# Kernel tuning notes

Measured on AMD Instinct MI355X. Metric: run time of the kernel, lower is better.

The kernel has to match this reference:

```python
import jax, jax.numpy as jnp
import numpy as np

EPS = 1e-5
GRID = 128          # coarse grid extent -> fine grid is 256^3
N1 = 15000          # coarse voxels
CHILD = 4           # children kept per coarse voxel
N2 = N1 * CHILD     # fine voxels
CIN = 128
COUT = 64


def _build_geometry():
    rng = np.random.RandomState(0)
    flat = rng.choice(GRID ** 3, N1, replace=False)
    cc = np.stack(np.unravel_index(flat, (GRID, GRID, GRID)), axis=1)  # [N1,3]
    offs8 = np.array([[i, j, k] for i in (0, 1) for j in (0, 1) for k in (0, 1)], dtype=np.int64)
    kidx = np.argsort(rng.rand(N1, 8), axis=1)[:, :CHILD]              # [N1,4] distinct child taps
    fine = (cc[:, None, :] * 2 + offs8[kidx]).reshape(-1, 3)           # [N2,3] unique fine coords
    up_src = np.repeat(np.arange(N1), CHILD).astype(np.int32)
    up_kidx = kidx.reshape(-1).astype(np.int32)
    # 27-offset neighbor maps via hashed coordinate lookup
    key = (fine[:, 0] * 256 + fine[:, 1]) * 256 + fine[:, 2]
    order = np.argsort(key)
    skey = key[order]
    offs27 = np.array([[i, j, k] for i in (-1, 0, 1) for j in (-1, 0, 1) for k in (-1, 0, 1)], dtype=np.int64)
    nbr_src = np.full((27, N2), N2, dtype=np.int32)
    nbr_dst = np.full((27, N2), N2, dtype=np.int32)
    for t in range(27):
        q = fine + offs27[t]
        inb = np.all((q >= 0) & (q < 256), axis=1)
        qk = (q[:, 0] * 256 + q[:, 1]) * 256 + q[:, 2]
        pos = np.searchsorted(skey, qk)
        pos = np.clip(pos, 0, N2 - 1)
        hit = inb & (skey[pos] == qk)
        nbr_src[t, hit] = order[pos[hit]]
        nbr_dst[t, hit] = np.arange(N2, dtype=np.int32)[hit]
    return up_src, up_kidx, nbr_src, nbr_dst


def setup_inputs() -> dict:
    key = jax.random.key(0)
    ks = jax.random.split(key, 8)
    up_src, up_kidx, nbr_src, nbr_dst = _build_geometry()
    s_up = 1.0 / np.sqrt(CIN * 8)
    s1 = 1.0 / np.sqrt(CIN * 27)
    s2 = 1.0 / np.sqrt(COUT * 27)
    return {
        "feats1": jax.random.normal(ks[0], (N1, CIN), jnp.float32),
        "feats2": jax.random.normal(ks[1], (N2, CIN // 2), jnp.float32),
        "w_up": jax.random.normal(ks[2], (8, CIN, CIN // 2), jnp.float32) * s_up,
        "gamma_up": jnp.ones((CIN // 2,), jnp.float32),
        "beta_up": jnp.zeros((CIN // 2,), jnp.float32),
        "w1": jax.random.normal(ks[3], (27, CIN, COUT), jnp.float32) * s1,
        "gamma1": jnp.ones((COUT,), jnp.float32),
        "beta1": jnp.zeros((COUT,), jnp.float32),
        "w2": jax.random.normal(ks[4], (27, COUT, COUT), jnp.float32) * s2,
        "gamma2": jnp.ones((COUT,), jnp.float32),
        "beta2": jnp.zeros((COUT,), jnp.float32),
        "up_src": jnp.asarray(up_src),
        "up_kidx": jnp.asarray(up_kidx),
        "nbr_src": jnp.asarray(nbr_src),
        "nbr_dst": jnp.asarray(nbr_dst),
    }


def _bn_relu(x, gamma, beta):
    # training-mode BatchNorm over the point dimension (biased variance), then ReLU
    m = jnp.mean(x, axis=0)
    v = jnp.var(x, axis=0)
    return jax.nn.relu((x - m) * jax.lax.rsqrt(v + EPS) * gamma + beta)


def _sparse_conv(x, w, nbr_src, nbr_dst):
    # x: [N,Ci]; w: [27,Ci,Co]; transform-then-gather-scatter (hash-map sparse conv)
    n = x.shape[0]
    co = w.shape[-1]
    y = jnp.einsum("nc,kco->kno", x, w)                       # [27,N,Co]
    y = jnp.concatenate([y, jnp.zeros((27, 1, co), y.dtype)], axis=1)  # sentinel row
    msg = jnp.take_along_axis(y, nbr_src[:, :, None], axis=1)  # [27,N,Co]
    out = jnp.zeros((n + 1, co), y.dtype).at[nbr_dst.reshape(-1)].add(msg.reshape(-1, co))
    return out[:-1]


def reference(feats1, feats2, w_up, gamma_up, beta_up, w1, gamma1, beta1, w2,
              gamma2, beta2, up_src, up_kidx, nbr_src, nbr_dst):
    # transposed conv k=2 s=2, generative=False: each fine voxel pulls from its unique coarse parent
    y = jnp.einsum("mc,kco->kmo", feats1, w_up)               # [8,N1,Cin/2]
    x1 = y[up_kidx, up_src]                                   # [N2,Cin/2]
    x1 = _bn_relu(x1, gamma_up, beta_up)
    x = jnp.concatenate([x1, feats2], axis=-1)                # [N2,Cin]
    h = _bn_relu(_sparse_conv(x, w1, nbr_src, nbr_dst), gamma1, beta1)
    return _bn_relu(_sparse_conv(h, w2, nbr_src, nbr_dst), gamma2, beta2)
```

## Files before the change

kernel.cpp:

```cpp
#include <hip/hip_runtime.h>


typedef short bf16x4 __attribute__((ext_vector_type(4)));
typedef short bf16x8 __attribute__((ext_vector_type(8)));
typedef float f32x16 __attribute__((ext_vector_type(16)));

__device__ __forceinline__ short f2bf(float f) {
    unsigned u = __float_as_uint(f);
    u += 0x7fffu + ((u >> 16) & 1u);
    return (short)(u >> 16);
}
__device__ __forceinline__ float bf2f(short s) {
    return __uint_as_float(((unsigned)(unsigned short)s) << 16);
}

__global__ __launch_bounds__(256) void k_setup(
    const float* __restrict__ w_up, const float* __restrict__ w1,
    const float* __restrict__ w2, const float* __restrict__ f1,
    const int* __restrict__ nbr, const int* __restrict__ up_kidx,
    short* __restrict__ wupp, short* __restrict__ w1p,
    short* __restrict__ w2p, short* __restrict__ f1bf,
    int* __restrict__ pmask, int* __restrict__ perm_rows,
    int* __restrict__ rank, int* __restrict__ cnt,
    int2* __restrict__ ext, int* __restrict__ extc,
    int n1, int n2, int nbExt, int nbGeom)
{
    int tid = threadIdx.x;
    int bid = blockIdx.x;
    if (bid < nbExt) {
        int i = bid * 256 + tid;
        unsigned hm = 0;
        if (i < n2) {
            #pragma unroll
            for (int t = 0; t < 27; ++t) {
                int s = nbr[(size_t)t * n2 + i];
                if (s < n2 && (s >> 2) != (i >> 2)) hm |= 1u << t;
            }
        }
        __shared__ int lcnt, lbase;
        if (tid == 0) lcnt = 0;
        __syncthreads();
        int nh = __popc(hm);
        int myofs = 0;
        if (nh) myofs = atomicAdd(&lcnt, nh);
        __syncthreads();
        if (tid == 0 && lcnt) lbase = atomicAdd(extc, lcnt);
        __syncthreads();
        if (nh) {
            int pos = lbase + myofs;
            unsigned m = hm;
            while (m) {
                int t = __ffs(m) - 1;
                m &= m - 1;
                int s = nbr[(size_t)t * n2 + i];
                ext[pos++] = make_int2(i, s | (t << 16));
            }
        }
    } else if (bid < nbExt + nbGeom) {
        int p = (bid - nbExt) * 256 + tid;
        if (p >= n1) return;
        int4 kd = *(const int4*)(up_kidx + 4 * p);
        int a = kd.x * 4 + 0, b = kd.y * 4 + 1, c = kd.z * 4 + 2, d = kd.w * 4 + 3;
        int t;
        if (a > b) { t = a; a = b; b = t; }
        if (c > d) { t = c; c = d; d = t; }
        if (a > c) { t = a; a = c; c = t; }
        if (b > d) { t = b; b = d; d = t; }
        if (b > c) { t = b; b = c; c = t; }
        perm_rows[4 * p + 0] = 4 * p + (a & 3);
        perm_rows[4 * p + 1] = 4 * p + (b & 3);
        perm_rows[4 * p + 2] = 4 * p + (c & 3);
        perm_rows[4 * p + 3] = 4 * p + (d & 3);
        int mask = (1 << (a >> 2)) | (1 << (b >> 2)) | (1 << (c >> 2)) | (1 << (d >> 2));
        pmask[p] = mask;
        rank[p] = atomicAdd(&cnt[mask], 1);
    } else {
        const long long nup = 65536, nw1 = 221184, nw2 = 110592;
        long long nf1 = (long long)n1 * 128;
        long long total = nup + nw1 + nw2 + nf1;
        long long gs = (long long)(gridDim.x - nbExt - nbGeom) * 256;
        for (long long e0 = (long long)(bid - nbExt - nbGeom) * 256 + tid;
             e0 < total; e0 += gs) {
            long long e = e0;
            if (e < nup) {
                int j = e & 7, l = (e >> 3) & 63, nt = (e >> 9) & 15, ks = (int)(e >> 13);
                int k = ks * 16 + (l >> 5) * 8 + j;
                int col = nt * 32 + (l & 31);
                wupp[e] = f2bf(w_up[((size_t)(col >> 6) * 128 + k) * 64 + (col & 63)]);
            } else if ((e -= nup) < nw1) {
                int j = e & 7, l = (e >> 3) & 63, ch = (e >> 9) & 1, ks = (e >> 10) & 7, t = (int)(e >> 13);
                int k = ks * 16 + (l >> 5) * 8 + j;
                int col = ch * 32 + (l & 31);
                w1p[e] = f2bf(w1[((size_t)t * 128 + k) * 64 + col]);
            } else if ((e -= nw1) < nw2) {
                int j = e & 7, l = (e >> 3) & 63, ch = (e >> 9) & 1, ks = (e >> 10) & 3, t = (int)(e >> 12);
                int k = ks * 16 + (l >> 5) * 8 + j;
                int col = ch * 32 + (l & 31);
                w2p[e] = f2bf(w2[((size_t)t * 64 + k) * 64 + col]);
            } else {
                e -= nw2;
                f1bf[e] = f2bf(f1[e]);
            }
        }
    }
}

__global__ __launch_bounds__(256) void k_up(
    const short* __restrict__ f1bf, const short* __restrict__ wupp,
    const int* __restrict__ pmask, const int* __restrict__ cnt,
    const int* __restrict__ rank, int* __restrict__ perm_par,
    int4* __restrict__ tiles, int* __restrict__ ntl,
    short* __restrict__ yup8, float* __restrict__ stats, int n1)
{
    if (blockIdx.x == 0) {
        __shared__ int sA[256], sB[256], bb[256];
        int t = threadIdx.x;
        int c = cnt[t], tc = (c + 31) >> 5;
        sA[t] = c; sB[t] = tc;
        __syncthreads();
        for (int off = 1; off < 256; off <<= 1) {
            int a = (t >= off) ? sA[t - off] : 0;
            int b = (t >= off) ? sB[t - off] : 0;
            __syncthreads();
            sA[t] += a; sB[t] += b;
            __syncthreads();
        }
        int base = sA[t] - c, toff = sB[t] - tc;
        bb[t] = base;
        for (int j = 0; j < tc; ++j) tiles[toff + j] = make_int4(t, base, j * 32, c);
        if (t == 255) ntl[0] = sB[255];
        __syncthreads();
        for (int p = t; p < n1; p += 256)
            perm_par[bb[pmask[p]] + rank[p]] = p;
        return;
    }
    __shared__ short lds[32 * 136];
    __shared__ float bs[64], bq[64];
    int bid = blockIdx.x - 1;
    int tile = bid >> 1;
    int w = threadIdx.x >> 6, lane = threadIdx.x & 63;
    int na = (bid & 1) * 8 + w, nb = na + 4;
    if (threadIdx.x < 64) { bs[threadIdx.x] = 0.f; bq[threadIdx.x] = 0.f; }
    #pragma unroll
    for (int it = 0; it < 2; ++it) {
        int c = it * 256 + threadIdx.x;
        int row = c >> 4, col8 = c & 15;
        int gr = tile * 32 + row; if (gr >= n1) gr = n1 - 1;
        int4 g = *(const int4*)(f1bf + (size_t)gr * 128 + col8 * 8);
        short* d = &lds[row * 136 + col8 * 8];
        *(int2*)d = make_int2(g.x, g.y);
        *(int2*)(d + 4) = make_int2(g.z, g.w);
    }
    int m = lane & 31, half = lane >> 5;
    int pm_l = (tile * 32 + m < n1) ? pmask[tile * 32 + m] : 0;
    __syncthreads();
    f32x16 a0, a1;
    #pragma unroll
    for (int i = 0; i < 16; ++i) { a0[i] = 0.f; a1[i] = 0.f; }
    const bf16x8* bp = (const bf16x8*)wupp;
    #pragma unroll
    for (int ks = 0; ks < 8; ++ks) {
        const short* ap = &lds[m * 136 + ks * 16 + half * 8];
        bf16x4 lo = *(const bf16x4*)ap, hi = *(const bf16x4*)(ap + 4);
        bf16x8 a = __builtin_shufflevector(lo, hi, 0, 1, 2, 3, 4, 5, 6, 7);
        bf16x8 b0 = bp[(size_t)(ks * 16 + na) * 64 + lane];
        bf16x8 b1 = bp[(size_t)(ks * 16 + nb) * 64 + lane];
        a0 = __builtin_amdgcn_mfma_f32_32x32x16_bf16(a, b0, a0, 0, 0, 0);
        a1 = __builtin_amdgcn_mfma_f32_32x32x16_bf16(a, b1, a1, 0, 0, 0);
    }
    int col = lane & 31;
    #pragma unroll
    for (int pass = 0; pass < 2; ++pass) {
        const f32x16& acc = pass ? a1 : a0;
        int n = pass ? nb : na;
        int slot = n >> 1, c = (n & 1) * 32 + col;
        float s0 = 0.f, q0 = 0.f;
        #pragma unroll
        for (int reg = 0; reg < 16; ++reg) {
            int r = (reg & 3) + 8 * (reg >> 2) + 4 * half;
            int p = tile * 32 + r;
            float v = acc[reg];
            int mk = __shfl(pm_l, r);
            if (p < n1) {
                yup8[(size_t)p * 512 + n * 32 + col] = f2bf(v);
                if ((mk >> slot) & 1) { s0 += v; q0 += v * v; }
            }
        }
        s0 += __shfl_xor(s0, 32);
        q0 += __shfl_xor(q0, 32);
        if (lane < 32) { atomicAdd(&bs[c], s0); atomicAdd(&bq[c], q0); }
    }
    __syncthreads();
    if (threadIdx.x < 64) {
        atomicAdd(&stats[threadIdx.x], bs[threadIdx.x]);
        atomicAdd(&stats[64 + threadIdx.x], bq[threadIdx.x]);
    }
}

__global__ __launch_bounds__(256) void k_extA(
    const short* __restrict__ yup8, const float* __restrict__ f2,
    const int* __restrict__ up_kidx, const float* __restrict__ w1,
    const float* __restrict__ gamma, const float* __restrict__ beta,
    const float* __restrict__ stats, const int2* __restrict__ ext,
    const int* __restrict__ extc, float* __restrict__ y,
    float* __restrict__ ostats, int n2)
{
    __shared__ float sc[64], sh[64], bs[64], bq[64];
    int tid = threadIdx.x;
    if (tid < 64) {
        float inv = 1.0f / (float)n2;
        float mean = stats[tid] * inv;
        float var = stats[64 + tid] * inv - mean * mean;
        float s = gamma[tid] * rsqrtf(var + 1e-5f);
        sc[tid] = s; sh[tid] = beta[tid] - mean * s;
        bs[tid] = 0.f; bq[tid] = 0.f;
    }
    __syncthreads();
    int gw = (blockIdx.x * 256 + tid) >> 6;
    int nw = (gridDim.x * 256) >> 6;
    int c = tid & 63;
    int ec = extc[0];
    float ls = 0.f, lq = 0.f;
    for (int e = gw; e < ec; e += nw) {
        int2 en = ext[e];
        int i = en.x, s = en.y & 0xFFFF, t = en.y >> 16;
        const short* xr = yup8 + (size_t)(s >> 2) * 512 + up_kidx[s] * 64;
        const float* fr = f2 + (size_t)s * 64;
        const float* wr = w1 + (size_t)t * 8192 + c;
        float acc = 0.f;
        #pragma unroll 4
        for (int k = 0; k < 64; ++k) {
            float xk = fmaxf(bf2f(xr[k]) * sc[k] + sh[k], 0.f);
            acc += xk * wr[(size_t)k * 64];
        }
        #pragma unroll 4
        for (int k = 0; k < 64; ++k)
            acc += fr[k] * wr[(size_t)(64 + k) * 64];
        float old = atomicAdd(&y[(size_t)i * 64 + c], acc);
        ls += acc;
        lq += acc * (2.f * old + acc);
    }
    atomicAdd(&bs[c], ls);
    atomicAdd(&bq[c], lq);
    __syncthreads();
    if (tid < 64) {
        atomicAdd(&ostats[tid], bs[tid]);
        atomicAdd(&ostats[64 + tid], bq[tid]);
    }
}

__global__ __launch_bounds__(256) void k_extB(
    const float* __restrict__ y1, const float* __restrict__ w2,
    const float* __restrict__ gamma, const float* __restrict__ beta,
    const float* __restrict__ stats, const int2* __restrict__ ext,
    const int* __restrict__ extc, float* __restrict__ y,
    float* __restrict__ ostats, int n2)
{
    __shared__ float sc[64], sh[64], bs[64], bq[64];
    int tid = threadIdx.x;
    if (tid < 64) {
        float inv = 1.0f / (float)n2;
        float mean = stats[tid] * inv;
        float var = stats[64 + tid] * inv - mean * mean;
        float s = gamma[tid] * rsqrtf(var + 1e-5f);
        sc[tid] = s; sh[tid] = beta[tid] - mean * s;
        bs[tid] = 0.f; bq[tid] = 0.f;
    }
    __syncthreads();
    int gw = (blockIdx.x * 256 + tid) >> 6;
    int nw = (gridDim.x * 256) >> 6;
    int c = tid & 63;
    int ec = extc[0];
    float ls = 0.f, lq = 0.f;
    for (int e = gw; e < ec; e += nw) {
        int2 en = ext[e];
        int i = en.x, s = en.y & 0xFFFF, t = en.y >> 16;
        const float* hr = y1 + (size_t)s * 64;
        const float* wr = w2 + (size_t)t * 4096 + c;
        float acc = 0.f;
        #pragma unroll 4
        for (int k = 0; k < 64; ++k) {
            float hk = fmaxf(hr[k] * sc[k] + sh[k], 0.f);
            acc += hk * wr[(size_t)k * 64];
        }
        float old = atomicAdd(&y[(size_t)i * 64 + c], acc);
        ls += acc;
        lq += acc * (2.f * old + acc);
    }
    atomicAdd(&bs[c], ls);
    atomicAdd(&bq[c], lq);
    __syncthreads();
    if (tid < 64) {
        atomicAdd(&ostats[tid], bs[tid]);
        atomicAdd(&ostats[64 + tid], bq[tid]);
    }
}

__device__ __forceinline__ void pair_epi_store(const f32x16& a0v, const f32x16& a1v,
                                               int outrow0, int outrow1, int lane,
                                               int ch, float* __restrict__ y,
                                               float* __restrict__ bs,
                                               float* __restrict__ bq)
{
    int col = lane & 31;
    int c = ch * 32 + col;
    int r0[16], r1[16];
    #pragma unroll
    for (int reg = 0; reg < 16; ++reg) {
        int r = (reg & 3) + 8 * (reg >> 2) + 4 * (lane >> 5);
        r0[reg] = __shfl(outrow0, r);
        r1[reg] = __shfl(outrow1, r);
    }
    float s0 = 0.f, q0 = 0.f;
    #pragma unroll
    for (int reg = 0; reg < 16; ++reg) {
        if (r0[reg] >= 0) {
            float v = a0v[reg];
            y[(size_t)r0[reg] * 64 + c] = v;
            s0 += v; q0 += v * v;
        }
        if (r1[reg] >= 0) {
            float v = a1v[reg];
            y[(size_t)r1[reg] * 64 + c] = v;
            s0 += v; q0 += v * v;
        }
    }
    s0 += __shfl_xor(s0, 32);
    q0 += __shfl_xor(q0, 32);
    if (lane < 32) { atomicAdd(&bs[c], s0); atomicAdd(&bq[c], q0); }
}

__device__ __forceinline__ int tap27(int pa, int pb) {
    int di = ((pb >> 2) & 1) - ((pa >> 2) & 1);
    int dj = ((pb >> 1) & 1) - ((pa >> 1) & 1);
    int dk = (pb & 1) - (pa & 1);
    return (di + 1) * 9 + (dj + 1) * 3 + (dk + 1);
}

__global__ __launch_bounds__(256) void k_pairA(
    const short* __restrict__ yup8, const float* __restrict__ f2,
    const int* __restrict__ up_kidx, const short* __restrict__ wp,
    const float* __restrict__ gamma, const float* __restrict__ beta,
    const float* __restrict__ stats, const int* __restrict__ perm_par,
    const int* __restrict__ perm_rows, const int4* __restrict__ tiles,
    const int* __restrict__ n_tiles, float* __restrict__ y,
    float* __restrict__ ostats, int n2)
{
    constexpr int LP = 520;
    __shared__ short lds[32 * LP];
    __shared__ int srows[128], soff[128];
    __shared__ float scs[64], shs[64], bs[64], bq[64];
    int bt = blockIdx.x;
    if (bt >= n_tiles[0]) return;
    int4 td = tiles[bt];
    int mask = td.x, p_start = td.y, lt = td.z, cntb = td.w;
    int tid = threadIdx.x;
    if (tid < 128) {
        int li = lt + (tid >> 2);
        int pid = perm_par[p_start + ((li < cntb) ? li : 0)];
        int i = perm_rows[pid * 4 + (tid & 3)];
        srows[tid] = i;
        soff[tid] = (i >> 2) * 512 + up_kidx[i] * 64;
    } else if (tid < 192) {
        int cc = tid - 128;
        float inv = 1.0f / (float)n2;
        float mean = stats[cc] * inv;
        float var = stats[64 + cc] * inv - mean * mean;
        float s = gamma[cc] * rsqrtf(var + 1e-5f);
        scs[cc] = s; shs[cc] = beta[cc] - mean * s;
    } else {
        int cc = tid - 192;
        bs[cc] = 0.f; bq[cc] = 0.f;
    }
    __syncthreads();
    #pragma unroll
    for (int it = 0; it < 8; ++it) {
        int c0 = it * 256 + tid;
        int pl = c0 >> 6, w8 = c0 & 63;
        int j = w8 >> 4, col8 = w8 & 15;
        short* d = &lds[pl * LP + j * 128 + col8 * 8];
        if (col8 < 8) {
            bf16x8 g = *(const bf16x8*)(yup8 + (size_t)soff[pl * 4 + j] + col8 * 8);
            short o[8];
            #pragma unroll
            for (int u = 0; u < 8; ++u) {
                int cc = col8 * 8 + u;
                o[u] = f2bf(fmaxf(bf2f(g[u]) * scs[cc] + shs[cc], 0.f));
            }
            *(int2*)d = make_int2(((int)(unsigned short)o[0]) | ((int)o[1] << 16),
                                  ((int)(unsigned short)o[2]) | ((int)o[3] << 16));
            *(int2*)(d + 4) = make_int2(((int)(unsigned short)o[4]) | ((int)o[5] << 16),
                                        ((int)(unsigned short)o[6]) | ((int)o[7] << 16));
        } else {
            const float* fr = f2 + (size_t)srows[pl * 4 + j] * 64 + (col8 - 8) * 8;
            float4 f0 = *(const float4*)fr;
            float4 f1v = *(const float4*)(fr + 4);
            short o[8] = {f2bf(f0.x), f2bf(f0.y), f2bf(f0.z), f2bf(f0.w),
                          f2bf(f1v.x), f2bf(f1v.y), f2bf(f1v.z), f2bf(f1v.w)};
            *(int2*)d = make_int2(((int)(unsigned short)o[0]) | ((int)o[1] << 16),
                                  ((int)(unsigned short)o[2]) | ((int)o[3] << 16));
            *(int2*)(d + 4) = make_int2(((int)(unsigned short)o[4]) | ((int)o[5] << 16),
                                        ((int)(unsigned short)o[6]) | ((int)o[7] << 16));
        }
    }
    int p0 = -1, p1 = -1, p2 = -1, p3 = -1;
    #pragma unroll
    for (int b = 7; b >= 0; --b)
        if ((mask >> b) & 1) { p3 = p2; p2 = p1; p1 = p0; p0 = b; }
    int w = tid >> 6, lane = tid & 63;
    int a0 = w >> 1, a1 = a0 + 2, ch = w & 1;
    int pa0 = (a0 == 0) ? p0 : p1;
    int pa1 = (a1 == 2) ? p2 : p3;
    int t00 = tap27(pa0, p0), t01 = tap27(pa0, p1), t02 = tap27(pa0, p2), t03 = tap27(pa0, p3);
    int t10 = tap27(pa1, p0), t11 = tap27(pa1, p1), t12 = tap27(pa1, p2), t13 = tap27(pa1, p3);
    int m = lane & 31, half = lane >> 5;
    int li = lt + m;
    bool vp = li < cntb;
    int pid = perm_par[p_start + (vp ? li : 0)];
    int outrow0 = vp ? perm_rows[pid * 4 + a0] : -1;
    int outrow1 = vp ? perm_rows[pid * 4 + a1] : -1;
    __syncthreads();
    f32x16 acc0, acc1;
    #pragma unroll
    for (int i = 0; i < 16; ++i) { acc0[i] = 0.f; acc1[i] = 0.f; }
    const bf16x8* bp = (const bf16x8*)wp;
    #pragma unroll
    for (int b = 0; b < 4; ++b) {
        int tb0 = (b == 0) ? t00 : (b == 1) ? t01 : (b == 2) ? t02 : t03;
        int tb1 = (b == 0) ? t10 : (b == 1) ? t11 : (b == 2) ? t12 : t13;
        #pragma unroll
        for (int kk = 0; kk < 8; ++kk) {
            int ks = b * 8 + kk;
            const short* ap = &lds[m * LP + ks * 16 + half * 8];
            bf16x4 lo = *(const bf16x4*)ap, hi = *(const bf16x4*)(ap + 4);
            bf16x8 a = __builtin_shufflevector(lo, hi, 0, 1, 2, 3, 4, 5, 6, 7);
            bf16x8 b0 = bp[((size_t)(tb0 * 8 + kk) * 2 + ch) * 64 + lane];
            bf16x8 b1 = bp[((size_t)(tb1 * 8 + kk) * 2 + ch) * 64 + lane];
            acc0 = __builtin_amdgcn_mfma_f32_32x32x16_bf16(a, b0, acc0, 0, 0, 0);
            acc1 = __builtin_amdgcn_mfma_f32_32x32x16_bf16(a, b1, acc1, 0, 0, 0);
        }
    }
    pair_epi_store(acc0, acc1, outrow0, outrow1, lane, ch, y, bs, bq);
    __syncthreads();
    if (tid < 64) {
        atomicAdd(&ostats[tid], bs[tid]);
        atomicAdd(&ostats[64 + tid], bq[tid]);
    }
}

__global__ __launch_bounds__(256) void k_pairB(
    const float* __restrict__ y1, const short* __restrict__ wp,
    const float* __restrict__ gamma, const float* __restrict__ beta,
    const float* __restrict__ stats, const int* __restrict__ perm_par,
    const int* __restrict__ perm_rows, const int4* __restrict__ tiles,
    const int* __restrict__ n_tiles, float* __restrict__ y,
    float* __restrict__ ostats, int n2)
{
    constexpr int LP = 264;
    __shared__ short lds[32 * LP];
    __shared__ int srows[128];
    __shared__ float scs[64], shs[64], bs[64], bq[64];
    int bt = blockIdx.x;
    if (bt >= n_tiles[0]) return;
    int4 td = tiles[bt];
    int mask = td.x, p_start = td.y, lt = td.z, cntb = td.w;
    int tid = threadIdx.x;
    if (tid < 128) {
        int li = lt + (tid >> 2);
        int pid = perm_par[p_start + ((li < cntb) ? li : 0)];
        srows[tid] = perm_rows[pid * 4 + (tid & 3)];
    } else if (tid < 192) {
        int cc = tid - 128;
        float inv = 1.0f / (float)n2;
        float mean = stats[cc] * inv;
        float var = stats[64 + cc] * inv - mean * mean;
        float s = gamma[cc] * rsqrtf(var + 1e-5f);
        scs[cc] = s; shs[cc] = beta[cc] - mean * s;
    } else {
        int cc = tid - 192;
        bs[cc] = 0.f; bq[cc] = 0.f;
    }
    __syncthreads();
    #pragma unroll
    for (int it = 0; it < 4; ++it) {
        int c0 = it * 256 + tid;
        int pl = c0 >> 5, w8 = c0 & 31;
        int j = w8 >> 3, col8 = w8 & 7;
        const float* fr = y1 + (size_t)srows[pl * 4 + j] * 64 + col8 * 8;
        float4 f0 = *(const float4*)fr;
        float4 f1v = *(const float4*)(fr + 4);
        short o[8];
        #pragma unroll
        for (int u = 0; u < 4; ++u) {
            int cc = col8 * 8 + u;
            float v = (u == 0) ? f0.x : (u == 1) ? f0.y : (u == 2) ? f0.z : f0.w;
            o[u] = f2bf(fmaxf(v * scs[cc] + shs[cc], 0.f));
        }
        #pragma unroll
        for (int u = 0; u < 4; ++u) {
            int cc = col8 * 8 + 4 + u;
            float v = (u == 0) ? f1v.x : (u == 1) ? f1v.y : (u == 2) ? f1v.z : f1v.w;
            o[4 + u] = f2bf(fmaxf(v * scs[cc] + shs[cc], 0.f));
        }
        short* d = &lds[pl * LP + j * 64 + col8 * 8];
        *(int2*)d = make_int2(((int)(unsigned short)o[0]) | ((int)o[1] << 16),
                              ((int)(unsigned short)o[2]) | ((int)o[3] << 16));
        *(int2*)(d + 4) = make_int2(((int)(unsigned short)o[4]) | ((int)o[5] << 16),
                                    ((int)(unsigned short)o[6]) | ((int)o[7] << 16));
    }
    int p0 = -1, p1 = -1, p2 = -1, p3 = -1;
    #pragma unroll
    for (int b = 7; b >= 0; --b)
        if ((mask >> b) & 1) { p3 = p2; p2 = p1; p1 = p0; p0 = b; }
    int w = tid >> 6, lane = tid & 63;
    int a0 = w >> 1, a1 = a0 + 2, ch = w & 1;
    int pa0 = (a0 == 0) ? p0 : p1;
    int pa1 = (a1 == 2) ? p2 : p3;
    int t00 = tap27(pa0, p0), t01 = tap27(pa0, p1), t02 = tap27(pa0, p2), t03 = tap27(pa0, p3);
    int t10 = tap27(pa1, p0), t11 = tap27(pa1, p1), t12 = tap27(pa1, p2), t13 = tap27(pa1, p3);
    int m = lane & 31, half = lane >> 5;
    int li = lt + m;
    bool vp = li < cntb;
    int pid = perm_par[p_start + (vp ? li : 0)];
    int outrow0 = vp ? perm_rows[pid * 4 + a0] : -1;
    int outrow1 = vp ? perm_rows[pid * 4 + a1] : -1;
    __syncthreads();
    f32x16 acc0, acc1;
    #pragma unroll
    for (int i = 0; i < 16; ++i) { acc0[i] = 0.f; acc1[i] = 0.f; }
    const bf16x8* bp = (const bf16x8*)wp;
    #pragma unroll
    for (int b = 0; b < 4; ++b) {
        int tb0 = (b == 0) ? t00 : (b == 1) ? t01 : (b == 2) ? t02 : t03;
        int tb1 = (b == 0) ? t10 : (b == 1) ? t11 : (b == 2) ? t12 : t13;
        #pragma unroll
        for (int kk = 0; kk < 4; ++kk) {
            int ks = b * 4 + kk;
            const short* ap = &lds[m * LP + ks * 16 + half * 8];
            bf16x4 lo = *(const bf16x4*)ap, hi = *(const bf16x4*)(ap + 4);
            bf16x8 a = __builtin_shufflevector(lo, hi, 0, 1, 2, 3, 4, 5, 6, 7);
            bf16x8 b0 = bp[((size_t)(tb0 * 4 + kk) * 2 + ch) * 64 + lane];
            bf16x8 b1 = bp[((size_t)(tb1 * 4 + kk) * 2 + ch) * 64 + lane];
            acc0 = __builtin_amdgcn_mfma_f32_32x32x16_bf16(a, b0, acc0, 0, 0, 0);
            acc1 = __builtin_amdgcn_mfma_f32_32x32x16_bf16(a, b1, acc1, 0, 0, 0);
        }
    }
    pair_epi_store(acc0, acc1, outrow0, outrow1, lane, ch, y, bs, bq);
    __syncthreads();
    if (tid < 64) {
        atomicAdd(&ostats[tid], bs[tid]);
        atomicAdd(&ostats[64 + tid], bq[tid]);
    }
}

__global__ __launch_bounds__(256) void k_final(
    const float* __restrict__ y, const float* __restrict__ gamma,
    const float* __restrict__ beta, const float* __restrict__ stats,
    float* __restrict__ out, int n2)
{
    __shared__ float sc[64], sh[64];
    int tid = threadIdx.x;
    if (tid < 64) {
        float inv = 1.0f / (float)n2;
        float mean = stats[tid] * inv;
        float var = stats[64 + tid] * inv - mean * mean;
        float s = gamma[tid] * rsqrtf(var + 1e-5f);
        sc[tid] = s;
        sh[tid] = beta[tid] - mean * s;
    }
    __syncthreads();
    long long total = (long long)n2 * 16;
    long long stride = (long long)gridDim.x * blockDim.x;
    for (long long idx = (long long)blockIdx.x * blockDim.x + tid; idx < total; idx += stride) {
        int i = (int)(idx >> 4);
        int c4 = ((int)idx & 15) * 4;
        const float* src = y + (size_t)i * 64 + c4;
        float4 o;
        o.x = fmaxf(src[0] * sc[c4 + 0] + sh[c4 + 0], 0.f);
        o.y = fmaxf(src[1] * sc[c4 + 1] + sh[c4 + 1], 0.f);
        o.z = fmaxf(src[2] * sc[c4 + 2] + sh[c4 + 2], 0.f);
        o.w = fmaxf(src[3] * sc[c4 + 3] + sh[c4 + 3], 0.f);
        *(float4*)(out + (size_t)i * 64 + c4) = o;
    }
}

extern "C" void kernel_launch(void* const* d_in, const int* in_sizes, int n_in,
                              void* d_out, int out_size, void* d_ws, size_t ws_size,
                              hipStream_t stream)
{
    const float* feats1   = (const float*)d_in[0];
    const float* feats2   = (const float*)d_in[1];
    const float* w_up     = (const float*)d_in[2];
    const float* gamma_up = (const float*)d_in[3];
    const float* beta_up  = (const float*)d_in[4];
    const float* w1       = (const float*)d_in[5];
    const float* gamma1   = (const float*)d_in[6];
    const float* beta1    = (const float*)d_in[7];
    const float* w2       = (const float*)d_in[8];
    const float* gamma2   = (const float*)d_in[9];
    const float* beta2    = (const float*)d_in[10];
    const int* up_kidx    = (const int*)d_in[12];
    const int* nbr_src    = (const int*)d_in[13];

    int n1 = in_sizes[0] / 128;
    int n2 = in_sizes[1] / 64;

    char* p = (char*)d_ws;
    auto alloc = [&](size_t bytes) {
        char* r = p;
        p += (bytes + 255) & ~(size_t)255;
        return r;
    };
    float* stats    = (float*)alloc(384 * 4);
    int*   cnt      = (int*)alloc(256 * 4);
    int*   extc     = (int*)alloc(16);
    int*   ntl      = (int*)alloc(16);
    size_t headBytes = (size_t)(p - (char*)d_ws);
    int maxTiles    = (n1 + 31) / 32 + 80;
    int4*  tiles    = (int4*)alloc((size_t)maxTiles * 16);
    short* wupp     = (short*)alloc((size_t)65536 * 2);
    short* w1p      = (short*)alloc((size_t)221184 * 2);
    short* w2p      = (short*)alloc((size_t)110592 * 2);
    short* f1bf     = (short*)alloc((size_t)n1 * 128 * 2);
    int*   pmask    = (int*)alloc((size_t)n1 * 4);
    int*   rank     = (int*)alloc((size_t)n1 * 4);
    int*   perm_par = (int*)alloc((size_t)n1 * 4);
    int*   perm_rows= (int*)alloc((size_t)4 * n1 * 4);
    int2*  ext      = (int2*)alloc((size_t)27 * n2 * 8);
    short* yup8     = (short*)alloc((size_t)n1 * 512 * 2);
    float* y1       = (float*)alloc((size_t)n2 * 64 * 4);
    float* y2       = (float*)alloc((size_t)n2 * 64 * 4);

    int nbExt  = (n2 + 255) / 256;
    int nbGeom = (n1 + 255) / 256;
    int nbPack = 256;
    int nbSetup = nbExt + nbGeom + nbPack;
    int upBlocks = 1 + 2 * ((n1 + 31) / 32);
    int ewBlocks16 = (int)(((long long)n2 * 16 + 255) / 256);

    hipMemsetAsync(d_ws, 0, headBytes, stream);
    k_setup<<<nbSetup, 256, 0, stream>>>(w_up, w1, w2, feats1, nbr_src, up_kidx,
                                         wupp, w1p, w2p, f1bf, pmask, perm_rows,
                                         rank, cnt, ext, extc, n1, n2,
                                         nbExt, nbGeom);
    k_up<<<upBlocks, 256, 0, stream>>>(f1bf, wupp, pmask, cnt, rank, perm_par,
                                       tiles, ntl, yup8, stats, n1);
    k_pairA<<<maxTiles, 256, 0, stream>>>(yup8, feats2, up_kidx, w1p, gamma_up,
                                          beta_up, stats, perm_par, perm_rows,
                                          tiles, ntl, y1, stats + 128, n2);
    k_extA<<<256, 256, 0, stream>>>(yup8, feats2, up_kidx, w1, gamma_up, beta_up,
                                    stats, ext, extc, y1, stats + 128, n2);
    k_pairB<<<maxTiles, 256, 0, stream>>>(y1, w2p, gamma1, beta1, stats + 128,
                                          perm_par, perm_rows, tiles, ntl, y2,
                                          stats + 256, n2);
    k_extB<<<256, 256, 0, stream>>>(y1, w2, gamma1, beta1, stats + 128, ext,
                                    extc, y2, stats + 256, n2);
    k_final<<<ewBlocks16, 256, 0, stream>>>(y2, gamma2, beta2, stats + 256,
                                            (float*)d_out, n2);
}
```

Baseline: 273.3 us.

## Merge pair-tile and cross-parent conv work into one launch per layer

Each sparse conv layer previously ran two kernels: an MFMA pair-tile kernel that stored outputs, then a scalar kernel that atomically added cross-parent contributions. Both now run as one grid, with extra blocks past the tile count doing the cross-parent work concurrently. Because of that, the tile epilogue switches from plain stores to atomicAdd into y1/y2, which are zero-filled in the setup kernel. Sum-of-squares stats are computed incrementally from the value returned by each atomic. This removes a launch and the serialization between the two parts per layer, at the cost of many more global atomics and extra zeroing traffic.

```diff
diff --git a/kernel.cpp b/kernel.cpp
--- a/kernel.cpp
+++ b/kernel.cpp
@@ -23,11 +23,18 @@
     int* __restrict__ pmask, int* __restrict__ perm_rows,
     int* __restrict__ rank, int* __restrict__ cnt,
     int2* __restrict__ ext, int* __restrict__ extc,
+    float* __restrict__ y1, float* __restrict__ y2,
     int n1, int n2, int nbExt, int nbGeom)
 {
     int tid = threadIdx.x;
     int bid = blockIdx.x;
     if (bid < nbExt) {
+        long long tot = (long long)n2 * 16;
+        long long gs = (long long)nbExt * 256;
+        for (long long e = (long long)bid * 256 + tid; e < tot; e += gs) {
+            ((float4*)y1)[e] = make_float4(0.f, 0.f, 0.f, 0.f);
+            ((float4*)y2)[e] = make_float4(0.f, 0.f, 0.f, 0.f);
+        }
         int i = bid * 256 + tid;
         unsigned hm = 0;
         if (i < n2) {
@@ -197,110 +204,11 @@
     }
 }
 
-__global__ __launch_bounds__(256) void k_extA(
-    const short* __restrict__ yup8, const float* __restrict__ f2,
-    const int* __restrict__ up_kidx, const float* __restrict__ w1,
-    const float* __restrict__ gamma, const float* __restrict__ beta,
-    const float* __restrict__ stats, const int2* __restrict__ ext,
-    const int* __restrict__ extc, float* __restrict__ y,
-    float* __restrict__ ostats, int n2)
-{
-    __shared__ float sc[64], sh[64], bs[64], bq[64];
-    int tid = threadIdx.x;
-    if (tid < 64) {
-        float inv = 1.0f / (float)n2;
-        float mean = stats[tid] * inv;
-        float var = stats[64 + tid] * inv - mean * mean;
-        float s = gamma[tid] * rsqrtf(var + 1e-5f);
-        sc[tid] = s; sh[tid] = beta[tid] - mean * s;
-        bs[tid] = 0.f; bq[tid] = 0.f;
-    }
-    __syncthreads();
-    int gw = (blockIdx.x * 256 + tid) >> 6;
-    int nw = (gridDim.x * 256) >> 6;
-    int c = tid & 63;
-    int ec = extc[0];
-    float ls = 0.f, lq = 0.f;
-    for (int e = gw; e < ec; e += nw) {
-        int2 en = ext[e];
-        int i = en.x, s = en.y & 0xFFFF, t = en.y >> 16;
-        const short* xr = yup8 + (size_t)(s >> 2) * 512 + up_kidx[s] * 64;
-        const float* fr = f2 + (size_t)s * 64;
-        const float* wr = w1 + (size_t)t * 8192 + c;
-        float acc = 0.f;
-        #pragma unroll 4
-        for (int k = 0; k < 64; ++k) {
-            float xk = fmaxf(bf2f(xr[k]) * sc[k] + sh[k], 0.f);
-            acc += xk * wr[(size_t)k * 64];
-        }
-        #pragma unroll 4
-        for (int k = 0; k < 64; ++k)
-            acc += fr[k] * wr[(size_t)(64 + k) * 64];
-        float old = atomicAdd(&y[(size_t)i * 64 + c], acc);
-        ls += acc;
-        lq += acc * (2.f * old + acc);
-    }
-    atomicAdd(&bs[c], ls);
-    atomicAdd(&bq[c], lq);
-    __syncthreads();
-    if (tid < 64) {
-        atomicAdd(&ostats[tid], bs[tid]);
-        atomicAdd(&ostats[64 + tid], bq[tid]);
-    }
-}
-
-__global__ __launch_bounds__(256) void k_extB(
-    const float* __restrict__ y1, const float* __restrict__ w2,
-    const float* __restrict__ gamma, const float* __restrict__ beta,
-    const float* __restrict__ stats, const int2* __restrict__ ext,
-    const int* __restrict__ extc, float* __restrict__ y,
-    float* __restrict__ ostats, int n2)
-{
-    __shared__ float sc[64], sh[64], bs[64], bq[64];
-    int tid = threadIdx.x;
-    if (tid < 64) {
-        float inv = 1.0f / (float)n2;
-        float mean = stats[tid] * inv;
-        float var = stats[64 + tid] * inv - mean * mean;
-        float s = gamma[tid] * rsqrtf(var + 1e-5f);
-        sc[tid] = s; sh[tid] = beta[tid] - mean * s;
-        bs[tid] = 0.f; bq[tid] = 0.f;
-    }
-    __syncthreads();
-    int gw = (blockIdx.x * 256 + tid) >> 6;
-    int nw = (gridDim.x * 256) >> 6;
-    int c = tid & 63;
-    int ec = extc[0];
-    float ls = 0.f, lq = 0.f;
-    for (int e = gw; e < ec; e += nw) {
-        int2 en = ext[e];
-        int i = en.x, s = en.y & 0xFFFF, t = en.y >> 16;
-        const float* hr = y1 + (size_t)s * 64;
-        const float* wr = w2 + (size_t)t * 4096 + c;
-        float acc = 0.f;
-        #pragma unroll 4
-        for (int k = 0; k < 64; ++k) {
-            float hk = fmaxf(hr[k] * sc[k] + sh[k], 0.f);
-            acc += hk * wr[(size_t)k * 64];
-        }
-        float old = atomicAdd(&y[(size_t)i * 64 + c], acc);
-        ls += acc;
-        lq += acc * (2.f * old + acc);
-    }
-    atomicAdd(&bs[c], ls);
-    atomicAdd(&bq[c], lq);
-    __syncthreads();
-    if (tid < 64) {
-        atomicAdd(&ostats[tid], bs[tid]);
-        atomicAdd(&ostats[64 + tid], bq[tid]);
-    }
-}
-
-__device__ __forceinline__ void pair_epi_store(const f32x16& a0v, const f32x16& a1v,
-                                               int outrow0, int outrow1, int lane,
-                                               int ch, float* __restrict__ y,
-                                               float* __restrict__ bs,
-                                               float* __restrict__ bq)
+__device__ __forceinline__ void pair_epi_at(const f32x16& a0v, const f32x16& a1v,
+                                            int outrow0, int outrow1, int lane,
+                                            int ch, float* __restrict__ y,
+                                            float* __restrict__ bs,
+                                            float* __restrict__ bq)
 {
     int col = lane & 31;
     int c = ch * 32 + col;
@@ -311,19 +219,17 @@
         r0[reg] = __shfl(outrow0, r);
         r1[reg] = __shfl(outrow1, r);
     }
+    float o0[16], o1[16];
+    #pragma unroll
+    for (int reg = 0; reg < 16; ++reg) {
+        o0[reg] = (r0[reg] >= 0) ? atomicAdd(&y[(size_t)r0[reg] * 64 + c], a0v[reg]) : 0.f;
+        o1[reg] = (r1[reg] >= 0) ? atomicAdd(&y[(size_t)r1[reg] * 64 + c], a1v[reg]) : 0.f;
+    }
     float s0 = 0.f, q0 = 0.f;
     #pragma unroll
     for (int reg = 0; reg < 16; ++reg) {
-        if (r0[reg] >= 0) {
-            float v = a0v[reg];
-            y[(size_t)r0[reg] * 64 + c] = v;
-            s0 += v; q0 += v * v;
-        }
-        if (r1[reg] >= 0) {
-            float v = a1v[reg];
-            y[(size_t)r1[reg] * 64 + c] = v;
-            s0 += v; q0 += v * v;
-        }
+        if (r0[reg] >= 0) { float d = a0v[reg]; s0 += d; q0 += d * (2.f * o0[reg] + d); }
+        if (r1[reg] >= 0) { float d = a1v[reg]; s0 += d; q0 += d * (2.f * o1[reg] + d); }
     }
     s0 += __shfl_xor(s0, 32);
     q0 += __shfl_xor(q0, 32);
@@ -337,24 +243,69 @@
     return (di + 1) * 9 + (dj + 1) * 3 + (dk + 1);
 }
 
-__global__ __launch_bounds__(256) void k_pairA(
+__global__ __launch_bounds__(256) void k_convA(
     const short* __restrict__ yup8, const float* __restrict__ f2,
     const int* __restrict__ up_kidx, const short* __restrict__ wp,
+    const float* __restrict__ w1f,
     const float* __restrict__ gamma, const float* __restrict__ beta,
     const float* __restrict__ stats, const int* __restrict__ perm_par,
     const int* __restrict__ perm_rows, const int4* __restrict__ tiles,
-    const int* __restrict__ n_tiles, float* __restrict__ y,
-    float* __restrict__ ostats, int n2)
+    const int* __restrict__ n_tiles, const int2* __restrict__ ext,
+    const int* __restrict__ extc, float* __restrict__ y,
+    float* __restrict__ ostats, int n2, int maxT)
 {
     constexpr int LP = 520;
     __shared__ short lds[32 * LP];
     __shared__ int srows[128], soff[128];
     __shared__ float scs[64], shs[64], bs[64], bq[64];
+    int tid = threadIdx.x;
+    if (blockIdx.x >= maxT) {
+        if (tid < 64) {
+            float inv = 1.0f / (float)n2;
+            float mean = stats[tid] * inv;
+            float var = stats[64 + tid] * inv - mean * mean;
+            float s = gamma[tid] * rsqrtf(var + 1e-5f);
+            scs[tid] = s; shs[tid] = beta[tid] - mean * s;
+            bs[tid] = 0.f; bq[tid] = 0.f;
+        }
+        __syncthreads();
+        int gw = ((blockIdx.x - maxT) * 256 + tid) >> 6;
+        int nw = ((gridDim.x - maxT) * 256) >> 6;
+        int c = tid & 63;
+        int ec = extc[0];
+        float ls = 0.f, lq = 0.f;
+        for (int e = gw; e < ec; e += nw) {
+            int2 en = ext[e];
+            int i = en.x, s = en.y & 0xFFFF, t = en.y >> 16;
+            const short* xr = yup8 + (size_t)(s >> 2) * 512 + up_kidx[s] * 64;
+            const float* fr = f2 + (size_t)s * 64;
+            const float* wr = w1f + (size_t)t * 8192 + c;
+            float acc = 0.f;
+            #pragma unroll 4
+            for (int k = 0; k < 64; ++k) {
+                float xk = fmaxf(bf2f(xr[k]) * scs[k] + shs[k], 0.f);
+                acc += xk * wr[(size_t)k * 64];
+            }
+            #pragma unroll 4
+            for (int k = 0; k < 64; ++k)
+                acc += fr[k] * wr[(size_t)(64 + k) * 64];
+            float old = atomicAdd(&y[(size_t)i * 64 + c], acc);
+            ls += acc;
+            lq += acc * (2.f * old + acc);
+        }
+        atomicAdd(&bs[c], ls);
+        atomicAdd(&bq[c], lq);
+        __syncthreads();
+        if (tid < 64) {
+            atomicAdd(&ostats[tid], bs[tid]);
+            atomicAdd(&ostats[64 + tid], bq[tid]);
+        }
+        return;
+    }
     int bt = blockIdx.x;
     if (bt >= n_tiles[0]) return;
     int4 td = tiles[bt];
     int mask = td.x, p_start = td.y, lt = td.z, cntb = td.w;
-    int tid = threadIdx.x;
     if (tid < 128) {
         int li = lt + (tid >> 2);
         int pid = perm_par[p_start + ((li < cntb) ? li : 0)];
@@ -440,7 +391,7 @@
             acc1 = __builtin_amdgcn_mfma_f32_32x32x16_bf16(a, b1, acc1, 0, 0, 0);
         }
     }
-    pair_epi_store(acc0, acc1, outrow0, outrow1, lane, ch, y, bs, bq);
+    pair_epi_at(acc0, acc1, outrow0, outrow1, lane, ch, y, bs, bq);
     __syncthreads();
     if (tid < 64) {
         atomicAdd(&ostats[tid], bs[tid]);
@@ -448,23 +399,64 @@
     }
 }
 
-__global__ __launch_bounds__(256) void k_pairB(
+__global__ __launch_bounds__(256) void k_convB(
     const float* __restrict__ y1, const short* __restrict__ wp,
+    const float* __restrict__ w2f,
     const float* __restrict__ gamma, const float* __restrict__ beta,
     const float* __restrict__ stats, const int* __restrict__ perm_par,
     const int* __restrict__ perm_rows, const int4* __restrict__ tiles,
-    const int* __restrict__ n_tiles, float* __restrict__ y,
-    float* __restrict__ ostats, int n2)
+    const int* __restrict__ n_tiles, const int2* __restrict__ ext,
+    const int* __restrict__ extc, float* __restrict__ y,
+    float* __restrict__ ostats, int n2, int maxT)
 {
     constexpr int LP = 264;
     __shared__ short lds[32 * LP];
     __shared__ int srows[128];
     __shared__ float scs[64], shs[64], bs[64], bq[64];
+    int tid = threadIdx.x;
+    if (blockIdx.x >= maxT) {
+        if (tid < 64) {
+            float inv = 1.0f / (float)n2;
+            float mean = stats[tid] * inv;
+            float var = stats[64 + tid] * inv - mean * mean;
+            float s = gamma[tid] * rsqrtf(var + 1e-5f);
+            scs[tid] = s; shs[tid] = beta[tid] - mean * s;
+            bs[tid] = 0.f; bq[tid] = 0.f;
+        }
+        __syncthreads();
+        int gw = ((blockIdx.x - maxT) * 256 + tid) >> 6;
+        int nw = ((gridDim.x - maxT) * 256) >> 6;
+        int c = tid & 63;
+        int ec = extc[0];
+        float ls = 0.f, lq = 0.f;
+        for (int e = gw; e < ec; e += nw) {
+            int2 en = ext[e];
+            int i = en.x, s = en.y & 0xFFFF, t = en.y >> 16;
+            const float* hr = y1 + (size_t)s * 64;
+            const float* wr = w2f + (size_t)t * 4096 + c;
+            float acc = 0.f;
+            #pragma unroll 4
+            for (int k = 0; k < 64; ++k) {
+                float hk = fmaxf(hr[k] * scs[k] + shs[k], 0.f);
+                acc += hk * wr[(size_t)k * 64];
+            }
+            float old = atomicAdd(&y[(size_t)i * 64 + c], acc);
+            ls += acc;
+            lq += acc * (2.f * old + acc);
+        }
+        atomicAdd(&bs[c], ls);
+        atomicAdd(&bq[c], lq);
+        __syncthreads();
+        if (tid < 64) {
+            atomicAdd(&ostats[tid], bs[tid]);
+            atomicAdd(&ostats[64 + tid], bq[tid]);
+        }
+        return;
+    }
     int bt = blockIdx.x;
     if (bt >= n_tiles[0]) return;
     int4 td = tiles[bt];
     int mask = td.x, p_start = td.y, lt = td.z, cntb = td.w;
-    int tid = threadIdx.x;
     if (tid < 128) {
         int li = lt + (tid >> 2);
         int pid = perm_par[p_start + ((li < cntb) ? li : 0)];
@@ -545,7 +537,7 @@
             acc1 = __builtin_amdgcn_mfma_f32_32x32x16_bf16(a, b1, acc1, 0, 0, 0);
         }
     }
-    pair_epi_store(acc0, acc1, outrow0, outrow1, lane, ch, y, bs, bq);
+    pair_epi_at(acc0, acc1, outrow0, outrow1, lane, ch, y, bs, bq);
     __syncthreads();
     if (tid < 64) {
         atomicAdd(&ostats[tid], bs[tid]);
@@ -636,25 +628,22 @@
     int nbPack = 256;
     int nbSetup = nbExt + nbGeom + nbPack;
     int upBlocks = 1 + 2 * ((n1 + 31) / 32);
+    int extBlk   = 128;
     int ewBlocks16 = (int)(((long long)n2 * 16 + 255) / 256);
 
     hipMemsetAsync(d_ws, 0, headBytes, stream);
     k_setup<<<nbSetup, 256, 0, stream>>>(w_up, w1, w2, feats1, nbr_src, up_kidx,
                                          wupp, w1p, w2p, f1bf, pmask, perm_rows,
-                                         rank, cnt, ext, extc, n1, n2,
-                                         nbExt, nbGeom);
+                                         rank, cnt, ext, extc, y1, y2,
+                                         n1, n2, nbExt, nbGeom);
     k_up<<<upBlocks, 256, 0, stream>>>(f1bf, wupp, pmask, cnt, rank, perm_par,
                                        tiles, ntl, yup8, stats, n1);
-    k_pairA<<<maxTiles, 256, 0, stream>>>(yup8, feats2, up_kidx, w1p, gamma_up,
-                                          beta_up, stats, perm_par, perm_rows,
-                                          tiles, ntl, y1, stats + 128, n2);
-    k_extA<<<256, 256, 0, stream>>>(yup8, feats2, up_kidx, w1, gamma_up, beta_up,
-                                    stats, ext, extc, y1, stats + 128, n2);
-    k_pairB<<<maxTiles, 256, 0, stream>>>(y1, w2p, gamma1, beta1, stats + 128,
-                                          perm_par, perm_rows, tiles, ntl, y2,
-                                          stats + 256, n2);
-    k_extB<<<256, 256, 0, stream>>>(y1, w2, gamma1, beta1, stats + 128, ext,
-                                    extc, y2, stats + 256, n2);
+    k_convA<<<maxTiles + extBlk, 256, 0, stream>>>(
+        yup8, feats2, up_kidx, w1p, w1, gamma_up, beta_up, stats, perm_par,
+        perm_rows, tiles, ntl, ext, extc, y1, stats + 128, n2, maxTiles);
+    k_convB<<<maxTiles + extBlk, 256, 0, stream>>>(
+        y1, w2p, w2, gamma1, beta1, stats + 128, perm_par, perm_rows, tiles,
+        ntl, ext, extc, y2, stats + 256, n2, maxTiles);
     k_final<<<ewBlocks16, 256, 0, stream>>>(y2, gamma2, beta2, stats + 256,
                                             (float*)d_out, n2);
 }
```

Measured after the change: 289.0 us. +5.7%, slower.
